# Performance work log

Hardware: AMD Instinct MI355X
Metric: run time of the kernel (lower is better)

The kernel has to match this reference:

```python
import jax, jax.numpy as jnp
import numpy as np

N_TOKEN = 4096
INPUT_DIM = 1024
QUERY_DIM = 1024
VALUE_DIM = 1024


def setup_inputs() -> dict:
    key = jax.random.key(0)
    ks = jax.random.split(key, 7)
    s = 0.02
    return {
        "x": jax.random.normal(ks[0], (N_TOKEN, INPUT_DIM), dtype=jnp.float32),
        "W_q": jax.random.normal(ks[1], (INPUT_DIM, QUERY_DIM), dtype=jnp.float32) * s,
        "b_q": jax.random.normal(ks[2], (QUERY_DIM,), dtype=jnp.float32) * s,
        "W_k": jax.random.normal(ks[3], (INPUT_DIM, QUERY_DIM), dtype=jnp.float32) * s,
        "b_k": jax.random.normal(ks[4], (QUERY_DIM,), dtype=jnp.float32) * s,
        "W_v": jax.random.normal(ks[5], (INPUT_DIM, VALUE_DIM), dtype=jnp.float32) * s,
        "b_v": jax.random.normal(ks[6], (VALUE_DIM,), dtype=jnp.float32) * s,
    }


def reference(x, W_q, b_q, W_k, b_k, W_v, b_v):
    # Projections: [n, d_in] @ [d_in, d_q/v]
    Q = x @ W_q + b_q
    K = x @ W_k + b_k
    V = x @ W_v + b_v
    n, q_dim = Q.shape
    scale = 1.0 / jnp.sqrt(jnp.asarray(q_dim, dtype=Q.dtype))
    scores = (Q @ K.T) * scale  # [n, n]
    # causal mask: positions j > i get -inf
    causal = jnp.tril(jnp.ones((n, n), dtype=bool))
    scores = jnp.where(causal, scores, -jnp.inf)
    attn = jax.nn.softmax(scores, axis=-1)
    return attn @ V
```

## Files before the change

kernel.cpp:

```cpp
#include <hip/hip_runtime.h>

#define N_TOK 4096
#define DIM   1024

typedef __bf16 bf16x8 __attribute__((ext_vector_type(8)));
typedef float  f32x4  __attribute__((ext_vector_type(4)));

__device__ __forceinline__ unsigned short f2bf(float f) {
  union { float f; unsigned u; } v; v.f = f;
  unsigned u = v.u;
  return (unsigned short)((u + 0x7fffu + ((u >> 16) & 1u)) >> 16);
}
__device__ __forceinline__ float bf2f(unsigned short h) {
  union { unsigned u; float f; } v; v.u = ((unsigned)h) << 16;
  return v.f;
}

__device__ __forceinline__ void gll16(const unsigned short* g,
                                      unsigned short* l) {
  __builtin_amdgcn_global_load_lds(
      (const __attribute__((address_space(1))) unsigned int*)g,
      (__attribute__((address_space(3))) unsigned int*)l, 16, 0, 0);
}

#define PB_CVT 0
#define PB_TQ 2048
#define PB_ZERO 5120
#define PB_LSUM 5888
#define PB_BIAS 5892
#define PB_TOTAL 5895

__global__ void prep(const float* __restrict__ x, const float* __restrict__ Wq,
                     const float* __restrict__ Wk, const float* __restrict__ Wv,
                     const float* __restrict__ bq, const float* __restrict__ bk,
                     const float* __restrict__ bv,
                     unsigned short* __restrict__ xb,
                     unsigned short* __restrict__ Wt,
                     float* __restrict__ out, float* __restrict__ ball,
                     float* __restrict__ Lsum) {
  const int b = blockIdx.x;
  const int t = threadIdx.x;
  if (b < PB_TQ) {
    const int i = ((b - PB_CVT) * 256 + t) * 8;
    float4 v0 = *(const float4*)(x + i);
    float4 v1 = *(const float4*)(x + i + 4);
    ushort4 r0, r1;
    r0.x = f2bf(v0.x); r0.y = f2bf(v0.y); r0.z = f2bf(v0.z); r0.w = f2bf(v0.w);
    r1.x = f2bf(v1.x); r1.y = f2bf(v1.y); r1.z = f2bf(v1.z); r1.w = f2bf(v1.w);
    *(ushort4*)(xb + i) = r0;
    *(ushort4*)(xb + i + 4) = r1;
  } else if (b < PB_ZERO) {
    const int which = (b - PB_TQ) >> 10;
    const int lb = (b - PB_TQ) & 1023;
    const float* W = (which == 0) ? Wq : (which == 1) ? Wk : Wv;
    unsigned short* D = Wt + (size_t)which * 1024 * 1024;
    __shared__ float tile[32][33];
    const int bx = (lb & 31) * 32, by = (lb >> 5) * 32;
    const int tx = t & 31, ty = t >> 5;
    for (int r = ty; r < 32; r += 8)
      tile[r][tx] = W[(size_t)(by + r) * DIM + bx + tx];
    __syncthreads();
    for (int r = ty; r < 32; r += 8)
      D[(size_t)(bx + r) * DIM + by + tx] = f2bf(tile[tx][r]);
  } else if (b < PB_LSUM) {
    float4* p = (float4*)(out + (size_t)1024 * DIM);
    const int i = ((b - PB_ZERO) * 256 + t) * 4;
#pragma unroll
    for (int c = 0; c < 4; c++) p[i + c] = make_float4(0.f, 0.f, 0.f, 0.f);
  } else if (b < PB_BIAS) {
    const int i = ((b - PB_LSUM) * 256 + t) * 4;
    *(float4*)(Lsum + i) = make_float4(0.f, 0.f, 0.f, 0.f);
  } else {
    const int i = ((b - PB_BIAS) * 256 + t) * 4;
#pragma unroll
    for (int c = 0; c < 4; c++) {
      const int k = i + c;
      if (k < 3072)
        ball[k] = (k < 1024) ? bq[k] * 0.03125f
                             : ((k < 2048) ? bk[k - 1024] : bv[k - 2048]);
    }
  }
}

__global__ void transpose_bf16(const unsigned short* __restrict__ V, int ldv,
                               unsigned short* __restrict__ Vt, int ldvt) {
  __shared__ unsigned short tile[32][33];
  int bx = blockIdx.x * 32;
  int by = blockIdx.y * 32;
  int tx = threadIdx.x, ty = threadIdx.y;
  for (int r = ty; r < 32; r += 8)
    tile[r][tx] = V[(size_t)(by + r) * ldv + bx + tx];
  __syncthreads();
  for (int r = ty; r < 32; r += 8)
    Vt[(size_t)(bx + r) * ldvt + by + tx] = tile[tx][r];
}

#define BK 64

template <int EPI>
__global__ __launch_bounds__(512, 2) void gemm_tn(
    const unsigned short* __restrict__ A, const unsigned short* __restrict__ B,
    void* __restrict__ Cout, const float* __restrict__ bias,
    float* __restrict__ Lsum, int K, int lda, int ldb, int ldc) {
  const int nwg = gridDim.x * gridDim.y;
  const int orig = blockIdx.y * gridDim.x + blockIdx.x;
  const int q8 = nwg >> 3, r8 = nwg & 7;
  const int xcd = orig & 7;
  const int wg = ((xcd < r8) ? xcd * (q8 + 1) : r8 * (q8 + 1) + (xcd - r8) * q8)
                 + (orig >> 3);
  int bm = wg / gridDim.x;
  int bn = wg % gridDim.x;

  int kbeg, kend;
  bool single = true;
  if (EPI == 3) {
    const int Keff = (bm + 1) * 256;
    kbeg = blockIdx.z * 1024;
    if (kbeg >= Keff) return;
    kend = min(kbeg + 1024, Keff);
    single = (Keff <= 1024);
  } else {
    if (EPI == 2 && bn > bm) return;
    kbeg = 0; kend = K;
  }

  __shared__ __align__(16) unsigned short smA[2][256 * 64];
  __shared__ __align__(16) unsigned short smB[2][256 * 64];

  const int t = threadIdx.x;
  const int lane = t & 63, w = t >> 6;
  const int wr = w >> 2;
  const int wc = w & 3;
  const int lane15 = lane & 15;
  const int kq = (lane >> 4) << 3;
  const int swz = (lane & 7) << 3;

  f32x4 acc[8][4] = {};

  const int lr = lane >> 3;
  const int g8 = ((lane & 7) ^ lr) << 3;
  const unsigned short* srcA =
      A + (size_t)((size_t)bm * 256 + (w << 4) + lr) * lda + g8 + kbeg;
  const unsigned short* srcB =
      B + (size_t)((size_t)bn * 256 + (w << 4) + lr) * ldb + g8 + kbeg;

  const int nt = (kend - kbeg) / BK;

  auto stg = [&](int bufi, int tt, int half) {
#pragma unroll
    for (int c = 0; c < 2; c++) {
      const int rb = half * 128 + (w << 4) + (c << 3);
      const size_t go = (size_t)(half * 128 + (c << 3));
      gll16(srcA + go * lda + (size_t)tt * BK, &smA[bufi][rb * 64]);
      gll16(srcB + go * ldb + (size_t)tt * BK, &smB[bufi][rb * 64]);
    }
  };

  stg(0, 0, 0);
  stg(0, 0, 1);
  asm volatile("s_waitcnt vmcnt(0)" ::: "memory");
  __builtin_amdgcn_s_barrier();

  int buf = 0;
  for (int tt = 0; tt < nt; ++tt) {
    const int nx = tt + 1;
    const unsigned short* sA = smA[buf];
    const unsigned short* sB = smB[buf];
    bf16x8 bA[4], bB0[4], bB1[4];
    const int kof0 = kq ^ swz;
    const int kof1 = (32 + kq) ^ swz;

#pragma unroll
    for (int i = 0; i < 4; i++)
      bA[i] = *(const bf16x8*)&sA[(wr * 128 + i * 16 + lane15) * 64 + kof0];
#pragma unroll
    for (int j = 0; j < 4; j++)
      bB0[j] = *(const bf16x8*)&sB[(wc * 64 + j * 16 + lane15) * 64 + kof0];
    if (nx < nt) stg(buf ^ 1, nx, 0);
    __builtin_amdgcn_s_barrier();
    asm volatile("s_waitcnt lgkmcnt(0)" ::: "memory");
    __builtin_amdgcn_s_setprio(1);
#pragma unroll
    for (int i = 0; i < 4; i++)
#pragma unroll
      for (int j = 0; j < 4; j++)
        acc[i][j] = __builtin_amdgcn_mfma_f32_16x16x32_bf16(bA[i], bB0[j],
                                                            acc[i][j], 0, 0, 0);
    __builtin_amdgcn_s_setprio(0);
    __builtin_amdgcn_s_barrier();

#pragma unroll
    for (int i = 0; i < 4; i++)
      bA[i] = *(const bf16x8*)&sA[(wr * 128 + i * 16 + lane15) * 64 + kof1];
#pragma unroll
    for (int j = 0; j < 4; j++)
      bB1[j] = *(const bf16x8*)&sB[(wc * 64 + j * 16 + lane15) * 64 + kof1];
    if (nx < nt) stg(buf ^ 1, nx, 1);
    __builtin_amdgcn_s_barrier();
    asm volatile("s_waitcnt lgkmcnt(0)" ::: "memory");
    __builtin_amdgcn_s_setprio(1);
#pragma unroll
    for (int i = 0; i < 4; i++)
#pragma unroll
      for (int j = 0; j < 4; j++)
        acc[i][j] = __builtin_amdgcn_mfma_f32_16x16x32_bf16(bA[i], bB1[j],
                                                            acc[i][j], 0, 0, 0);
    __builtin_amdgcn_s_setprio(0);
    __builtin_amdgcn_s_barrier();

#pragma unroll
    for (int i = 0; i < 4; i++)
      bA[i] = *(const bf16x8*)&sA[(wr * 128 + 64 + i * 16 + lane15) * 64 + kof0];
    __builtin_amdgcn_s_barrier();
    asm volatile("s_waitcnt lgkmcnt(0)" ::: "memory");
    __builtin_amdgcn_s_setprio(1);
#pragma unroll
    for (int i = 0; i < 4; i++)
#pragma unroll
      for (int j = 0; j < 4; j++)
        acc[4 + i][j] = __builtin_amdgcn_mfma_f32_16x16x32_bf16(
            bA[i], bB0[j], acc[4 + i][j], 0, 0, 0);
    __builtin_amdgcn_s_setprio(0);
    __builtin_amdgcn_s_barrier();

#pragma unroll
    for (int i = 0; i < 4; i++)
      bA[i] = *(const bf16x8*)&sA[(wr * 128 + 64 + i * 16 + lane15) * 64 + kof1];
    __builtin_amdgcn_s_barrier();
    asm volatile("s_waitcnt lgkmcnt(0)" ::: "memory");
    __builtin_amdgcn_s_setprio(1);
#pragma unroll
    for (int i = 0; i < 4; i++)
#pragma unroll
      for (int j = 0; j < 4; j++)
        acc[4 + i][j] = __builtin_amdgcn_mfma_f32_16x16x32_bf16(
            bA[i], bB1[j], acc[4 + i][j], 0, 0, 0);
    __builtin_amdgcn_s_setprio(0);
    if (nx < nt) asm volatile("s_waitcnt vmcnt(0)" ::: "memory");
    __builtin_amdgcn_s_barrier();
    buf ^= 1;
  }

  float* Cf = (float*)Cout;
  unsigned short* Ch = (unsigned short*)Cout;
  const int colbase = bn * 256 + wc * 64 + lane15;
  const int rowbase = bm * 256 + wr * 128 + ((lane >> 4) << 2);

  if (EPI == 0) {
#pragma unroll
    for (int i = 0; i < 8; i++)
#pragma unroll
      for (int j = 0; j < 4; j++) {
        const int gc = colbase + j * 16;
        const float cs = (gc < 1024) ? 0.03125f : 1.0f;
        const float bs = bias[gc];
#pragma unroll
        for (int r = 0; r < 4; r++) {
          const int gr = rowbase + i * 16 + r;
          Ch[(size_t)gr * ldc + gc] = f2bf(acc[i][j][r] * cs + bs);
        }
      }
  } else if (EPI == 2) {
    __syncthreads();
    float* Lp = (float*)smA;
    if (t < 256) Lp[t] = 0.f;
    __syncthreads();
#pragma unroll
    for (int i = 0; i < 8; i++)
#pragma unroll
      for (int r = 0; r < 4; r++) {
        const int gr = rowbase + i * 16 + r;
        float sj = 0.f;
#pragma unroll
        for (int j = 0; j < 4; j++) {
          const int gc = colbase + j * 16;
          unsigned short h = 0;
          if (gc <= gr) h = f2bf(__expf(acc[i][j][r]));
          Ch[(size_t)gr * ldc + gc] = h;
          sj += bf2f(h);
        }
        sj += __shfl_xor(sj, 1);
        sj += __shfl_xor(sj, 2);
        sj += __shfl_xor(sj, 4);
        sj += __shfl_xor(sj, 8);
        if (lane15 == 0)
          atomicAdd(&Lp[wr * 128 + i * 16 + ((lane >> 4) << 2) + r], sj);
      }
    __syncthreads();
    if (t < 256) atomicAdd(&Lsum[bm * 256 + t], Lp[t]);
  } else {
#pragma unroll
    for (int i = 0; i < 8; i++)
#pragma unroll
      for (int r = 0; r < 4; r++) {
        const int gr = rowbase + i * 16 + r;
        const float linv = 1.0f / Lsum[gr];
#pragma unroll
        for (int j = 0; j < 4; j++) {
          const int gc = colbase + j * 16;
          const float v = acc[i][j][r] * linv;
          if (single)
            Cf[(size_t)gr * ldc + gc] = v;
          else
            atomicAdd(&Cf[(size_t)gr * ldc + gc], v);
        }
      }
  }
}

extern "C" void kernel_launch(void* const* d_in, const int* in_sizes, int n_in,
                              void* d_out, int out_size, void* d_ws,
                              size_t ws_size, hipStream_t stream) {
  (void)in_sizes; (void)n_in; (void)out_size; (void)ws_size;
  const float* x  = (const float*)d_in[0];
  const float* Wq = (const float*)d_in[1];
  const float* bq = (const float*)d_in[2];
  const float* Wk = (const float*)d_in[3];
  const float* bk = (const float*)d_in[4];
  const float* Wv = (const float*)d_in[5];
  const float* bv = (const float*)d_in[6];
  float* out = (float*)d_out;

  const size_t M1 = (size_t)1024 * 1024;
  unsigned short* xb   = (unsigned short*)d_ws;
  unsigned short* Wt   = xb + 4 * M1;
  unsigned short* Call = Wt + 3 * M1;
  unsigned short* Sb   = Call + 12 * M1;
  float* ball          = (float*)(Sb + 16 * M1);
  float* Lsum          = ball + 3072;

  prep<<<PB_TOTAL, 256, 0, stream>>>(x, Wq, Wk, Wv, bq, bk, bv, xb, Wt, out,
                                     ball, Lsum);
  gemm_tn<0><<<dim3(12, 16), 512, 0, stream>>>(xb, Wt, Call, ball, nullptr,
                                               DIM, DIM, DIM, 3 * DIM);
  transpose_bf16<<<dim3(32, 128), dim3(32, 8), 0, stream>>>(Call + 2048,
                                                            3 * DIM, xb, N_TOK);
  gemm_tn<2><<<dim3(16, 16), 512, 0, stream>>>(Call, Call + 1024, Sb, nullptr,
                                               Lsum, DIM, 3 * DIM, 3 * DIM,
                                               N_TOK);
  gemm_tn<3><<<dim3(4, 16, 4), 512, 0, stream>>>(Sb, xb, out, nullptr, Lsum,
                                                 N_TOK, N_TOK, N_TOK, DIM);
}
```

Measured before the change: 227.3 us.

## Reorder GEMM tile staging for partial vmcnt waits and double split-K for PV

The shared-memory staging of each K tile is reorganised. All of B plus the first half of A's rows is loaded in an alpha phase, and the second half of A in a beta phase. Waits become partial vmcnt counts, so the second half of A can still be in flight while the first MFMA block computes, and the trailing per-iteration vmcnt(0) and barrier are removed. Separately, the attention-times-V GEMM split-K chunk shrinks from 1024 to 512 with twice the z-grid, and the prep zeroing of the output is widened to match. This adds parallelism on the causal triangle at the cost of more atomic or accumulation traffic into the output.

```diff
diff --git a/kernel.cpp b/kernel.cpp
--- a/kernel.cpp
+++ b/kernel.cpp
@@ -26,9 +26,9 @@
 #define PB_CVT 0
 #define PB_TQ 2048
 #define PB_ZERO 5120
-#define PB_LSUM 5888
-#define PB_BIAS 5892
-#define PB_TOTAL 5895
+#define PB_LSUM 6016
+#define PB_BIAS 6020
+#define PB_TOTAL 6023
 
 __global__ void prep(const float* __restrict__ x, const float* __restrict__ Wq,
                      const float* __restrict__ Wk, const float* __restrict__ Wv,
@@ -63,7 +63,7 @@
     for (int r = ty; r < 32; r += 8)
       D[(size_t)(bx + r) * DIM + by + tx] = f2bf(tile[tx][r]);
   } else if (b < PB_LSUM) {
-    float4* p = (float4*)(out + (size_t)1024 * DIM);
+    float4* p = (float4*)(out + (size_t)512 * DIM);
     const int i = ((b - PB_ZERO) * 256 + t) * 4;
 #pragma unroll
     for (int c = 0; c < 4; c++) p[i + c] = make_float4(0.f, 0.f, 0.f, 0.f);
@@ -115,10 +115,10 @@
   bool single = true;
   if (EPI == 3) {
     const int Keff = (bm + 1) * 256;
-    kbeg = blockIdx.z * 1024;
+    kbeg = blockIdx.z * 512;
     if (kbeg >= Keff) return;
-    kend = min(kbeg + 1024, Keff);
-    single = (Keff <= 1024);
+    kend = min(kbeg + 512, Keff);
+    single = (Keff <= 512);
   } else {
     if (EPI == 2 && bn > bm) return;
     kbeg = 0; kend = K;
@@ -139,36 +139,46 @@
 
   const int lr = lane >> 3;
   const int g8 = ((lane & 7) ^ lr) << 3;
-  const unsigned short* srcA =
-      A + (size_t)((size_t)bm * 256 + (w << 4) + lr) * lda + g8 + kbeg;
-  const unsigned short* srcB =
-      B + (size_t)((size_t)bn * 256 + (w << 4) + lr) * ldb + g8 + kbeg;
+  const unsigned short* gA =
+      A + (size_t)((size_t)bm * 256 + lr) * lda + g8 + kbeg;
+  const unsigned short* gB =
+      B + (size_t)((size_t)bn * 256 + lr) * ldb + g8 + kbeg;
+
+  const int bB = w << 5;
+  const int a0 = ((w & 3) << 4) + ((w >> 2) << 7);
 
   const int nt = (kend - kbeg) / BK;
 
-  auto stg = [&](int bufi, int tt, int half) {
-#pragma unroll
-    for (int c = 0; c < 2; c++) {
-      const int rb = half * 128 + (w << 4) + (c << 3);
-      const size_t go = (size_t)(half * 128 + (c << 3));
-      gll16(srcA + go * lda + (size_t)tt * BK, &smA[bufi][rb * 64]);
-      gll16(srcB + go * ldb + (size_t)tt * BK, &smB[bufi][rb * 64]);
-    }
+  auto stgAlpha = [&](int bufi, int tt) {
+    const size_t ko = (size_t)tt * BK;
+#pragma unroll
+    for (int c = 0; c < 4; c++)
+      gll16(gB + (size_t)(bB + (c << 3)) * ldb + ko,
+            &smB[bufi][(bB + (c << 3)) * 64]);
+    gll16(gA + (size_t)a0 * lda + ko, &smA[bufi][a0 * 64]);
+    gll16(gA + (size_t)(a0 + 8) * lda + ko, &smA[bufi][(a0 + 8) * 64]);
   };
-
-  stg(0, 0, 0);
-  stg(0, 0, 1);
-  asm volatile("s_waitcnt vmcnt(0)" ::: "memory");
-  __builtin_amdgcn_s_barrier();
+  auto stgBeta = [&](int bufi, int tt) {
+    const size_t ko = (size_t)tt * BK;
+    gll16(gA + (size_t)(a0 + 64) * lda + ko, &smA[bufi][(a0 + 64) * 64]);
+    gll16(gA + (size_t)(a0 + 72) * lda + ko, &smA[bufi][(a0 + 72) * 64]);
+  };
+
+  stgAlpha(0, 0);
+  stgBeta(0, 0);
 
   int buf = 0;
   for (int tt = 0; tt < nt; ++tt) {
     const int nx = tt + 1;
     const unsigned short* sA = smA[buf];
     const unsigned short* sB = smB[buf];
-    bf16x8 bA[4], bB0[4], bB1[4];
     const int kof0 = kq ^ swz;
     const int kof1 = (32 + kq) ^ swz;
+    bf16x8 bA[4], bB0[4], bB1[4];
+
+    asm volatile("s_waitcnt vmcnt(2)" ::: "memory");
+    __builtin_amdgcn_s_barrier();
+    __builtin_amdgcn_sched_barrier(0);
 
 #pragma unroll
     for (int i = 0; i < 4; i++)
@@ -176,7 +186,7 @@
 #pragma unroll
     for (int j = 0; j < 4; j++)
       bB0[j] = *(const bf16x8*)&sB[(wc * 64 + j * 16 + lane15) * 64 + kof0];
-    if (nx < nt) stg(buf ^ 1, nx, 0);
+    if (nx < nt) stgAlpha(buf ^ 1, nx);
     __builtin_amdgcn_s_barrier();
     asm volatile("s_waitcnt lgkmcnt(0)" ::: "memory");
     __builtin_amdgcn_s_setprio(1);
@@ -195,7 +205,7 @@
 #pragma unroll
     for (int j = 0; j < 4; j++)
       bB1[j] = *(const bf16x8*)&sB[(wc * 64 + j * 16 + lane15) * 64 + kof1];
-    if (nx < nt) stg(buf ^ 1, nx, 1);
+    if (nx < nt) stgBeta(buf ^ 1, nx);
     __builtin_amdgcn_s_barrier();
     asm volatile("s_waitcnt lgkmcnt(0)" ::: "memory");
     __builtin_amdgcn_s_setprio(1);
@@ -206,6 +216,11 @@
         acc[i][j] = __builtin_amdgcn_mfma_f32_16x16x32_bf16(bA[i], bB1[j],
                                                             acc[i][j], 0, 0, 0);
     __builtin_amdgcn_s_setprio(0);
+    if (nx < nt) {
+      asm volatile("s_waitcnt vmcnt(8)" ::: "memory");
+    } else {
+      asm volatile("s_waitcnt vmcnt(0)" ::: "memory");
+    }
     __builtin_amdgcn_s_barrier();
 
 #pragma unroll
@@ -236,8 +251,6 @@
         acc[4 + i][j] = __builtin_amdgcn_mfma_f32_16x16x32_bf16(
             bA[i], bB1[j], acc[4 + i][j], 0, 0, 0);
     __builtin_amdgcn_s_setprio(0);
-    if (nx < nt) asm volatile("s_waitcnt vmcnt(0)" ::: "memory");
-    __builtin_amdgcn_s_barrier();
     buf ^= 1;
   }
 
@@ -338,6 +351,6 @@
   gemm_tn<2><<<dim3(16, 16), 512, 0, stream>>>(Call, Call + 1024, Sb, nullptr,
                                                Lsum, DIM, 3 * DIM, 3 * DIM,
                                                N_TOK);
-  gemm_tn<3><<<dim3(4, 16, 4), 512, 0, stream>>>(Sb, xb, out, nullptr, Lsum,
+  gemm_tn<3><<<dim3(4, 16, 8), 512, 0, stream>>>(Sb, xb, out, nullptr, Lsum,
                                                  N_TOK, N_TOK, N_TOK, DIM);
 }
```

After: 262.3 us. 15.4% more time.
